# Kernel optimization log

Measured on AMD Instinct MI355X. Metric: run time of the kernel, lower is better.

## Reference

```python
import jax, jax.numpy as jnp
import numpy as np

OUT_FEATURES = 14336
IN_FEATURES = 4096
BITS = 4
MAX_INT = (1 << (BITS - 1)) - 1  # 7


def setup_inputs() -> dict:
    key = jax.random.key(0)
    kx, kw, kb = jax.random.split(key, 3)
    x = jax.random.normal(kx, (4, 2048, IN_FEATURES), dtype=jnp.float32)
    # materialize a float weight, then quantize exactly like the torch __init__
    weight = jax.random.normal(kw, (OUT_FEATURES, IN_FEATURES), dtype=jnp.float32) * 0.02
    scale = jnp.abs(weight).max(axis=1) / MAX_INT  # per-row scale [O]
    q = jnp.clip(jnp.round(weight / scale[:, None]), -MAX_INT - 1, MAX_INT).astype(jnp.int32)
    # pack two int4 values per int8: even nibble high, odd nibble low
    even, odd = q[:, 0::2], q[:, 1::2]
    qweight = ((even << 4) | (odd & 15)).astype(jnp.int8)  # [O, I//2]
    bias = jax.random.normal(kb, (OUT_FEATURES,), dtype=jnp.float32) * 0.01
    return {"x": x, "qweight": qweight, "scale": scale, "bias": bias}


def _dequant4(qweight, scale):
    w = qweight.astype(jnp.int32)
    high = w >> 4  # arithmetic shift, sign-extended high nibble
    low = ((w & 15) ^ 8) - 8  # sign-extended low nibble
    unpacked = jnp.stack([high, low], axis=-1).reshape(qweight.shape[0], -1)  # [O, I]
    unpacked = unpacked[:, :IN_FEATURES]
    return unpacked.astype(jnp.float32) * scale[:, None]


def reference(x, qweight, scale, bias):
    w_deq = _dequant4(qweight, scale)  # [O, I] fp32
    out = jnp.einsum("bsi,oi->bso", x.astype(jnp.float32), w_deq)
    out = out + bias.astype(jnp.float32)
    return out.astype(x.dtype)
```

## Files before the change

### kernel.cpp

```cpp
#include <hip/hip_runtime.h>
#include <stdint.h>

#define M_DIM 8192
#define N_DIM 14336
#define K_DIM 4096

typedef __bf16 bf16x8 __attribute__((ext_vector_type(8)));
typedef float f32x4 __attribute__((ext_vector_type(4)));
typedef uint16_t u16x8 __attribute__((ext_vector_type(8)));


__device__ __forceinline__ uint16_t f2bf(float f) {
  union { float f; uint32_t u; } v; v.f = f;
  uint32_t u = v.u;
  return (uint16_t)((u + 0x7FFFu + ((u >> 16) & 1u)) >> 16);
}

__device__ __forceinline__ void load_lds16(const void* g, void* l) {
  __builtin_amdgcn_global_load_lds(
      (const __attribute__((address_space(1))) uint32_t*)g,
      (__attribute__((address_space(3))) uint32_t*)l,
      16, 0, 0);
}


__global__ __launch_bounds__(256) void cvt_x_kernel(const float4* __restrict__ x,
                                                    u16x8* __restrict__ out, int n) {
  int i = blockIdx.x * 256 + threadIdx.x;
  if (i >= n) return;
  float4 a = x[2 * i], b = x[2 * i + 1];
  u16x8 r;
  r[0] = f2bf(a.x); r[1] = f2bf(a.y); r[2] = f2bf(a.z); r[3] = f2bf(a.w);
  r[4] = f2bf(b.x); r[5] = f2bf(b.y); r[6] = f2bf(b.z); r[7] = f2bf(b.w);
  out[i] = r;
}


__global__ __launch_bounds__(256) void dequant_w_kernel(const int4* __restrict__ qw,
                                                        u16x8* __restrict__ out, int n) {
  int i = blockIdx.x * 256 + threadIdx.x;
  if (i >= n) return;
  int4 p = qw[i];
  int v[4] = {p.x, p.y, p.z, p.w};
  u16x8 r;
#pragma unroll
  for (int b = 0; b < 4; b++) {
    int byte = (int)(int8_t)(v[b] & 0xFF);
    int hi = byte >> 4;
    int lo = ((byte & 15) ^ 8) - 8;
    r[2 * b]     = f2bf((float)hi);
    r[2 * b + 1] = f2bf((float)lo);
  }
  out[i] = r;
}


__global__ __launch_bounds__(256, 2) void gemm_bt_kernel(
    const uint16_t* __restrict__ A, const uint16_t* __restrict__ B,
    const float* __restrict__ scale, const float* __restrict__ bias,
    float* __restrict__ C) {
  constexpr int BM = 128, BN = 128, BK = 32;
  constexpr int NT = N_DIM / BN;

  __shared__ alignas(16) uint16_t As[BM * BK];
  __shared__ alignas(16) uint16_t Bs[BN * BK];

  const int tid = threadIdx.x;
  const int lane = tid & 63;
  const int wave = tid >> 6;
  const int bm = blockIdx.x / NT;
  const int bn = blockIdx.x % NT;
  const int mBase = bm * BM, nBase = bn * BN;
  const int waveM = (wave >> 1) * 64, waveN = (wave & 1) * 64;

  f32x4 acc[4][4] = {};

  const int c0 = wave * 2, c1 = wave * 2 + 1;
  const int r0 = c0 * 16 + (lane >> 2);
  const int r1 = c1 * 16 + (lane >> 2);
  const int kof = (lane & 3) * 8;
  const uint16_t* gA = A + (size_t)mBase * K_DIM;
  const uint16_t* gB = B + (size_t)nBase * K_DIM;

  const int kf = (lane >> 4) * 8;
  const int rm = lane & 15;

  for (int k0 = 0; k0 < K_DIM; k0 += BK) {
    load_lds16(gA + (size_t)r0 * K_DIM + k0 + kof, &As[c0 * 512]);
    load_lds16(gA + (size_t)r1 * K_DIM + k0 + kof, &As[c1 * 512]);
    load_lds16(gB + (size_t)r0 * K_DIM + k0 + kof, &Bs[c0 * 512]);
    load_lds16(gB + (size_t)r1 * K_DIM + k0 + kof, &Bs[c1 * 512]);
    __syncthreads();

    bf16x8 af[4], bfr[4];
#pragma unroll
    for (int mi = 0; mi < 4; mi++)
      af[mi] = *(const bf16x8*)&As[(waveM + mi * 16 + rm) * BK + kf];
#pragma unroll
    for (int ni = 0; ni < 4; ni++)
      bfr[ni] = *(const bf16x8*)&Bs[(waveN + ni * 16 + rm) * BK + kf];

#pragma unroll
    for (int mi = 0; mi < 4; mi++)
#pragma unroll
      for (int ni = 0; ni < 4; ni++)
        acc[mi][ni] = __builtin_amdgcn_mfma_f32_16x16x32_bf16(af[mi], bfr[ni], acc[mi][ni], 0, 0, 0);

    __syncthreads();
  }

#pragma unroll
  for (int ni = 0; ni < 4; ni++) {
    const int cg = nBase + waveN + ni * 16 + rm;
    const float s = scale[cg];
    const float bb = bias[cg];
#pragma unroll
    for (int mi = 0; mi < 4; mi++) {
      const int rg = mBase + waveM + mi * 16 + (lane >> 4) * 4;
#pragma unroll
      for (int r = 0; r < 4; r++)
        C[(size_t)(rg + r) * N_DIM + cg] = acc[mi][ni][r] * s + bb;
    }
  }
}


__global__ __launch_bounds__(256) void fallback_kernel(
    const float* __restrict__ x, const int* __restrict__ qw,
    const float* __restrict__ scale, const float* __restrict__ bias,
    float* __restrict__ out) {
  int n = blockIdx.x * 256 + threadIdx.x;
  int m = blockIdx.y;
  const int* wr = qw + (size_t)n * (K_DIM / 2);
  const float* xr = x + (size_t)m * K_DIM;
  float acc = 0.f;
  for (int j = 0; j < K_DIM / 2; j++) {
    int byte = (int)(int8_t)(wr[j] & 0xFF);
    int hi = byte >> 4;
    int lo = ((byte & 15) ^ 8) - 8;
    acc += xr[2 * j] * (float)hi + xr[2 * j + 1] * (float)lo;
  }
  out[(size_t)m * N_DIM + n] = acc * scale[n] + bias[n];
}


extern "C" void kernel_launch(void* const* d_in, const int* in_sizes, int n_in,
                              void* d_out, int out_size, void* d_ws, size_t ws_size,
                              hipStream_t stream) {
  const float* x = (const float*)d_in[0];
  const int* qw = (const int*)d_in[1];
  const float* scale = (const float*)d_in[2];
  const float* bias = (const float*)d_in[3];
  float* out = (float*)d_out;

  const size_t xb_bytes = (size_t)M_DIM * K_DIM * 2;
  const size_t wb_bytes = (size_t)N_DIM * K_DIM * 2;

  if (ws_size < xb_bytes + wb_bytes) {
    dim3 g(N_DIM / 256, M_DIM);
    fallback_kernel<<<g, 256, 0, stream>>>(x, qw, scale, bias, out);
    return;
  }

  uint16_t* xb = (uint16_t*)d_ws;
  uint16_t* wb = (uint16_t*)((char*)d_ws + xb_bytes);

  const int n8x = M_DIM * K_DIM / 8;
  cvt_x_kernel<<<dim3(n8x / 256), 256, 0, stream>>>((const float4*)x, (u16x8*)xb, n8x);

  const int n4w = N_DIM * K_DIM / 8;
  dequant_w_kernel<<<dim3(n4w / 256), 256, 0, stream>>>((const int4*)qw, (u16x8*)wb, n4w);

  gemm_bt_kernel<<<dim3((M_DIM / 128) * (N_DIM / 128)), 256, 0, stream>>>(
      xb, wb, scale, bias, out);
}
```

Measured before the change: 1.852 ms.

## Replace GEMM with 256x256 double-buffered pipelined kernel using swizzled LDS

Replaces the 128x128, BK=32 single-buffered GEMM with a 256x256-tile, 512-thread kernel. It uses BK=64, double-buffered LDS and an XOR-swizzled LDS layout, and interleaves async global-to-LDS loads with MFMA quadrants under manual barriers and wait counts. It also remaps block IDs so each XCD handles nearby M tiles for L2 reuse, and uses nontemporal output stores. The goal is to hide memory latency, cut LDS bank conflicts and raise arithmetic intensity. In exchange it needs 128KB of LDS and much more register pressure, and its correctness depends on the hand-written synchronization.

Result: faster. 1.618 ms (-12.6%).

```diff
diff --git a/kernel.cpp b/kernel.cpp
--- a/kernel.cpp
+++ b/kernel.cpp
@@ -55,71 +55,137 @@
 }
 
 
-__global__ __launch_bounds__(256, 2) void gemm_bt_kernel(
+#define SBAR      asm volatile("s_barrier" ::: "memory")
+#define LGKM0     do { asm volatile("s_waitcnt lgkmcnt(0)" ::: "memory"); \
+                       __builtin_amdgcn_sched_barrier(0); } while (0)
+#define VMCNT(n_) asm volatile("s_waitcnt vmcnt(" #n_ ")" ::: "memory")
+
+#define RD_A(b_, kh_, mi_) \
+  af[kh_][mi_] = *(const bf16x8*)(ldsA + (b_) * 32768 + ((kh_) ? aoff1 : aoff0) + (mi_) * 2048)
+#define RD_B(b_, kh_, ni_) \
+  bfr[kh_][ni_] = *(const bf16x8*)(ldsB + (b_) * 32768 + ((kh_) ? boff1 : boff0) + (ni_) * 2048)
+
+#define STGA(b_, u_, kt2_) \
+  load_lds16(gA + (size_t)((u_) * 64 + trow) * K_DIM + (size_t)(kt2_) * 64 + tslot * 8, \
+             &As[b_][(u_) * 64 + (wave << 3)][0])
+#define STGB(b_, u_, kt2_) \
+  load_lds16(gB + (size_t)((u_) * 64 + trow) * K_DIM + (size_t)(kt2_) * 64 + tslot * 8, \
+             &Bs[b_][(u_) * 64 + (wave << 3)][0])
+
+#define MM(kh_, mi_, ni_) \
+  acc[mi_][ni_] = __builtin_amdgcn_mfma_f32_16x16x32_bf16(af[kh_][mi_], bfr[kh_][ni_], acc[mi_][ni_], 0, 0, 0)
+#define MQ(qm_, qn_) do { \
+  MM(0,(qm_)*4+0,(qn_)*2+0); MM(1,(qm_)*4+0,(qn_)*2+0); \
+  MM(0,(qm_)*4+1,(qn_)*2+0); MM(1,(qm_)*4+1,(qn_)*2+0); \
+  MM(0,(qm_)*4+2,(qn_)*2+0); MM(1,(qm_)*4+2,(qn_)*2+0); \
+  MM(0,(qm_)*4+3,(qn_)*2+0); MM(1,(qm_)*4+3,(qn_)*2+0); \
+  MM(0,(qm_)*4+0,(qn_)*2+1); MM(1,(qm_)*4+0,(qn_)*2+1); \
+  MM(0,(qm_)*4+1,(qn_)*2+1); MM(1,(qm_)*4+1,(qn_)*2+1); \
+  MM(0,(qm_)*4+2,(qn_)*2+1); MM(1,(qm_)*4+2,(qn_)*2+1); \
+  MM(0,(qm_)*4+3,(qn_)*2+1); MM(1,(qm_)*4+3,(qn_)*2+1); \
+} while (0)
+
+#define TILE(kt_, B_) do { \
+  const int ktn_  = ((kt_) + 1 < NKT) ? (kt_) + 1 : NKT - 1; \
+  const int ktn2_ = ((kt_) + 2 < NKT) ? (kt_) + 2 : NKT - 1; \
+   \
+  RD_A(B_,0,0); RD_A(B_,1,0); RD_A(B_,0,1); RD_A(B_,1,1); \
+  RD_A(B_,0,2); RD_A(B_,1,2); RD_A(B_,0,3); RD_A(B_,1,3); \
+  RD_B(B_,0,0); RD_B(B_,1,0); RD_B(B_,0,1); RD_B(B_,1,1); \
+  STGA((B_)^1, 0, ktn_); STGA((B_)^1, 2, ktn_); \
+  SBAR; LGKM0; \
+  __builtin_amdgcn_s_setprio(1); MQ(0,0); __builtin_amdgcn_s_setprio(0); \
+  SBAR; \
+   \
+  RD_A(B_,0,4); RD_A(B_,1,4); RD_A(B_,0,5); RD_A(B_,1,5); \
+  RD_A(B_,0,6); RD_A(B_,1,6); RD_A(B_,0,7); RD_A(B_,1,7); \
+  RD_B(B_,0,2); RD_B(B_,1,2); RD_B(B_,0,3); RD_B(B_,1,3); \
+  STGA((B_)^1, 1, ktn_); STGA((B_)^1, 3, ktn_); \
+  SBAR; LGKM0; \
+  __builtin_amdgcn_s_setprio(1); MQ(1,1); __builtin_amdgcn_s_setprio(0); \
+  SBAR; \
+   \
+  STGB(B_, 0, ktn2_); STGB(B_, 1, ktn2_); \
+  SBAR; \
+  __builtin_amdgcn_s_setprio(1); MQ(1,0); __builtin_amdgcn_s_setprio(0); \
+  SBAR; \
+   \
+  STGB(B_, 2, ktn2_); STGB(B_, 3, ktn2_); \
+  SBAR; \
+  __builtin_amdgcn_s_setprio(1); MQ(0,1); __builtin_amdgcn_s_setprio(0); \
+  VMCNT(4); \
+  SBAR; \
+} while (0)
+
+__global__ __launch_bounds__(512, 2) void gemm256_kernel(
     const uint16_t* __restrict__ A, const uint16_t* __restrict__ B,
     const float* __restrict__ scale, const float* __restrict__ bias,
     float* __restrict__ C) {
-  constexpr int BM = 128, BN = 128, BK = 32;
-  constexpr int NT = N_DIM / BN;
-
-  __shared__ alignas(16) uint16_t As[BM * BK];
-  __shared__ alignas(16) uint16_t Bs[BN * BK];
+  constexpr int NKT = K_DIM / 64;
+  static_assert(M_DIM % 256 == 0 && N_DIM % 256 == 0 && (NKT % 2) == 0, "shape");
+
+  __shared__ alignas(16) uint16_t As[2][256][64];
+  __shared__ alignas(16) uint16_t Bs[2][256][64];
 
   const int tid = threadIdx.x;
   const int lane = tid & 63;
   const int wave = tid >> 6;
-  const int bm = blockIdx.x / NT;
-  const int bn = blockIdx.x % NT;
-  const int mBase = bm * BM, nBase = bn * BN;
-  const int waveM = (wave >> 1) * 64, waveN = (wave & 1) * 64;
-
-  f32x4 acc[4][4] = {};
-
-  const int c0 = wave * 2, c1 = wave * 2 + 1;
-  const int r0 = c0 * 16 + (lane >> 2);
-  const int r1 = c1 * 16 + (lane >> 2);
-  const int kof = (lane & 3) * 8;
+  const int wm = wave >> 2;
+  const int wn = wave & 3;
+
+  const int orig = blockIdx.x;
+  const int xcd = orig & 7;
+  const int local = orig >> 3;
+  const int bm = xcd * 4 + (local & 3);
+  const int bn = local >> 2;
+  const int mBase = bm * 256, nBase = bn * 256;
+
   const uint16_t* gA = A + (size_t)mBase * K_DIM;
   const uint16_t* gB = B + (size_t)nBase * K_DIM;
 
-  const int kf = (lane >> 4) * 8;
-  const int rm = lane & 15;
-
-  for (int k0 = 0; k0 < K_DIM; k0 += BK) {
-    load_lds16(gA + (size_t)r0 * K_DIM + k0 + kof, &As[c0 * 512]);
-    load_lds16(gA + (size_t)r1 * K_DIM + k0 + kof, &As[c1 * 512]);
-    load_lds16(gB + (size_t)r0 * K_DIM + k0 + kof, &Bs[c0 * 512]);
-    load_lds16(gB + (size_t)r1 * K_DIM + k0 + kof, &Bs[c1 * 512]);
-    __syncthreads();
-
-    bf16x8 af[4], bfr[4];
-#pragma unroll
-    for (int mi = 0; mi < 4; mi++)
-      af[mi] = *(const bf16x8*)&As[(waveM + mi * 16 + rm) * BK + kf];
-#pragma unroll
-    for (int ni = 0; ni < 4; ni++)
-      bfr[ni] = *(const bf16x8*)&Bs[(waveN + ni * 16 + rm) * BK + kf];
-
-#pragma unroll
-    for (int mi = 0; mi < 4; mi++)
-#pragma unroll
-      for (int ni = 0; ni < 4; ni++)
-        acc[mi][ni] = __builtin_amdgcn_mfma_f32_16x16x32_bf16(af[mi], bfr[ni], acc[mi][ni], 0, 0, 0);
-
-    __syncthreads();
-  }
-
-#pragma unroll
-  for (int ni = 0; ni < 4; ni++) {
-    const int cg = nBase + waveN + ni * 16 + rm;
+  const int trow = tid >> 3;
+  const int tslot = (tid & 7) ^ (trow & 7);
+
+  const int fr = lane & 15;
+  const int fc = lane >> 4;
+  const int s7 = fr & 7;
+  const int aoff0 = (wm * 128 + fr) * 128 + ((fc    ) ^ s7) * 16;
+  const int aoff1 = (wm * 128 + fr) * 128 + ((fc + 4) ^ s7) * 16;
+  const int boff0 = (wn * 64 + fr) * 128 + ((fc    ) ^ s7) * 16;
+  const int boff1 = (wn * 64 + fr) * 128 + ((fc + 4) ^ s7) * 16;
+  const char* ldsA = (const char*)As;
+  const char* ldsB = (const char*)Bs;
+
+  bf16x8 af[2][8], bfr[2][4];
+  f32x4 acc[8][4] = {};
+
+  STGB(0, 0, 0); STGB(0, 1, 0); STGB(0, 2, 0); STGB(0, 3, 0);
+  STGA(0, 0, 0); STGA(0, 2, 0);
+  STGA(0, 1, 0); STGA(0, 3, 0);
+  STGB(1, 0, 1); STGB(1, 1, 1); STGB(1, 2, 1); STGB(1, 3, 1);
+  VMCNT(4);
+  SBAR;
+
+#pragma unroll 1
+  for (int kt = 0; kt < NKT; kt += 2) {
+    TILE(kt, 0);
+    TILE(kt + 1, 1);
+  }
+
+  asm volatile("s_waitcnt vmcnt(0)" ::: "memory");
+
+#pragma unroll
+  for (int ni = 0; ni < 4; ++ni) {
+    const int cg = nBase + wn * 64 + ni * 16 + fr;
     const float s = scale[cg];
     const float bb = bias[cg];
 #pragma unroll
-    for (int mi = 0; mi < 4; mi++) {
-      const int rg = mBase + waveM + mi * 16 + (lane >> 4) * 4;
-#pragma unroll
-      for (int r = 0; r < 4; r++)
-        C[(size_t)(rg + r) * N_DIM + cg] = acc[mi][ni][r] * s + bb;
+    for (int mi = 0; mi < 8; ++mi) {
+      const size_t rg = (size_t)(mBase + wm * 128 + mi * 16 + fc * 4);
+#pragma unroll
+      for (int r = 0; r < 4; ++r)
+        __builtin_nontemporal_store(acc[mi][ni][r] * s + bb,
+                                    &C[(rg + r) * N_DIM + cg]);
     }
   }
 }
@@ -171,6 +237,6 @@
   const int n4w = N_DIM * K_DIM / 8;
   dequant_w_kernel<<<dim3(n4w / 256), 256, 0, stream>>>((const int4*)qw, (u16x8*)wb, n4w);
 
-  gemm_bt_kernel<<<dim3((M_DIM / 128) * (N_DIM / 128)), 256, 0, stream>>>(
+  gemm256_kernel<<<dim3((M_DIM / 256) * (N_DIM / 256)), 512, 0, stream>>>(
       xb, wb, scale, bias, out);
 }
```
